# Kernel optimization log

Measured on AMD Instinct MI355X. Metric: run time of the kernel, lower is better.

## Reference

```python
import jax, jax.numpy as jnp
import numpy as np
import math

D_MODEL, N_HEADS, D_FF = 1024, 16, 4096
D_K = D_MODEL // N_HEADS
B, S = 4, 2048
EPS = 1e-5


def layer_norm(x, gamma, beta):
    mean = jnp.mean(x, axis=-1, keepdims=True)
    var = jnp.mean((x - mean) ** 2, axis=-1, keepdims=True)  # unbiased=False
    return gamma * (x - mean) / jnp.sqrt(var + EPS) + beta


def setup_inputs() -> dict:
    key = jax.random.key(0)
    ks = jax.random.split(key, 7)
    std_attn = math.sqrt(2.0 / (D_MODEL + D_MODEL))
    std_ff1 = math.sqrt(2.0 / (D_MODEL + D_FF))
    std_ff2 = math.sqrt(2.0 / (D_FF + D_MODEL))
    return {
        "x": jax.random.normal(ks[0], (B, S, D_MODEL), jnp.float32),
        "W_q": jax.random.normal(ks[1], (D_MODEL, D_MODEL), jnp.float32) * std_attn,
        "W_k": jax.random.normal(ks[2], (D_MODEL, D_MODEL), jnp.float32) * std_attn,
        "W_v": jax.random.normal(ks[3], (D_MODEL, D_MODEL), jnp.float32) * std_attn,
        "W_o": jax.random.normal(ks[4], (D_MODEL, D_MODEL), jnp.float32) * std_attn,
        "W1": jax.random.normal(ks[5], (D_MODEL, D_FF), jnp.float32) * std_ff1,
        "b1": jnp.zeros((D_FF,), jnp.float32),
        "W2": jax.random.normal(ks[6], (D_FF, D_MODEL), jnp.float32) * std_ff2,
        "b2": jnp.zeros((D_MODEL,), jnp.float32),
        "ln1_gamma": jnp.ones((D_MODEL,), jnp.float32),
        "ln1_beta": jnp.zeros((D_MODEL,), jnp.float32),
        "ln2_gamma": jnp.ones((D_MODEL,), jnp.float32),
        "ln2_beta": jnp.zeros((D_MODEL,), jnp.float32),
    }


def reference(x, W_q, W_k, W_v, W_o, W1, b1, W2, b2,
              ln1_gamma, ln1_beta, ln2_gamma, ln2_beta):
    b, s, d = x.shape
    # pre-LN attention block
    ln1 = layer_norm(x, ln1_gamma, ln1_beta)
    q = (ln1 @ W_q).reshape(b, s, N_HEADS, D_K)
    k = (ln1 @ W_k).reshape(b, s, N_HEADS, D_K)
    v = (ln1 @ W_v).reshape(b, s, N_HEADS, D_K)
    scores = jnp.einsum("bqhd,bkhd->bhqk", q, k) / math.sqrt(D_K)
    attn = jax.nn.softmax(scores, axis=-1)
    ctx = jnp.einsum("bhqk,bkhd->bqhd", attn, v).reshape(b, s, d)
    attn_out = ctx @ W_o
    attn_residual = x + attn_out
    # pre-LN FFN block
    ln2 = layer_norm(attn_residual, ln2_gamma, ln2_beta)
    ff = jax.nn.relu(ln2 @ W1 + b1) @ W2 + b2
    return attn_residual + ff
```

## Files before the change

kernel.cpp:

```cpp
#include <hip/hip_runtime.h>
#include <hip/hip_bf16.h>

typedef __attribute__((ext_vector_type(4))) float  floatx4;
typedef __attribute__((ext_vector_type(8))) short  shortx8;
typedef __attribute__((ext_vector_type(4))) short  shortx4;

__device__ __forceinline__ short f2bf(float f) {
    unsigned u = __float_as_uint(f);
    u += 0x7fffu + ((u >> 16) & 1u);
    return (short)(u >> 16);
}
__device__ __forceinline__ float bf2f(short s) {
    return __uint_as_float(((unsigned)(unsigned short)s) << 16);
}
__device__ __forceinline__ float fast_exp2(float x) {
#if __has_builtin(__builtin_amdgcn_exp2f)
    return __builtin_amdgcn_exp2f(x);
#else
    return exp2f(x);
#endif
}

__device__ __forceinline__ void load_lds16(const void* g, void* l) {
    __builtin_amdgcn_global_load_lds(
        (const __attribute__((address_space(1))) unsigned int*)g,
        (__attribute__((address_space(3))) unsigned int*)l,
        16, 0, 0);
}

__global__ __launch_bounds__(256)
void transpose_w(const float* __restrict__ src, short* __restrict__ dst, int K, int N)
{
    __shared__ __align__(16) float tile[32][33];
    const int n0 = blockIdx.x * 32, k0 = blockIdx.y * 32;
    const int tx = threadIdx.x & 31, ty = threadIdx.x >> 5;
    for (int i = 0; i < 32; i += 8)
        tile[ty + i][tx] = src[(size_t)(k0 + ty + i) * N + n0 + tx];
    __syncthreads();
    for (int i = 0; i < 32; i += 8)
        dst[(size_t)(n0 + ty + i) * K + k0 + tx] = f2bf(tile[tx][ty + i]);
}

__global__ __launch_bounds__(256)
void ln_bf16(const float* __restrict__ x, const float* __restrict__ g,
             const float* __restrict__ be, short* __restrict__ out)
{
    const int row = blockIdx.x;
    const int tid = threadIdx.x;
    const float4 v = reinterpret_cast<const float4*>(x + (size_t)row * 1024)[tid];
    float s  = v.x + v.y + v.z + v.w;
    float ss = v.x * v.x + v.y * v.y + v.z * v.z + v.w * v.w;
    for (int off = 32; off > 0; off >>= 1) {
        s  += __shfl_down(s,  off);
        ss += __shfl_down(ss, off);
    }
    __shared__ float rs[4], rss[4];
    const int wave = tid >> 6, lane = tid & 63;
    if (lane == 0) { rs[wave] = s; rss[wave] = ss; }
    __syncthreads();
    const float S    = rs[0] + rs[1] + rs[2] + rs[3];
    const float SS   = rss[0] + rss[1] + rss[2] + rss[3];
    const float mean = S * (1.0f / 1024.0f);
    const float var  = SS * (1.0f / 1024.0f) - mean * mean;
    const float rstd = rsqrtf(var + 1e-5f);
    const float4 gg = reinterpret_cast<const float4*>(g)[tid];
    const float4 bb = reinterpret_cast<const float4*>(be)[tid];
    shortx4 o;
    o[0] = f2bf(gg.x * ((v.x - mean) * rstd) + bb.x);
    o[1] = f2bf(gg.y * ((v.y - mean) * rstd) + bb.y);
    o[2] = f2bf(gg.z * ((v.z - mean) * rstd) + bb.z);
    o[3] = f2bf(gg.w * ((v.w - mean) * rstd) + bb.w);
    *reinterpret_cast<shortx4*>(out + (size_t)row * 1024 + tid * 4) = o;
}

template <int EPI>
__global__ __launch_bounds__(256)
void gemm_bt(const short* __restrict__ A, const short* __restrict__ Bt,
             short* __restrict__ Cb, float* __restrict__ Cf,
             const float* __restrict__ bias, const float* __restrict__ resid,
             int M, int N, int K)
{
    __shared__ __align__(16) short As[128 * 32];
    __shared__ __align__(16) short Bs[128 * 32];
    const int tid  = threadIdx.x;
    const int wave = tid >> 6;
    const int lane = tid & 63;
    const int quad = lane >> 4;
    const int l16  = lane & 15;
    const int wm = wave >> 1, wn = wave & 1;
    const size_t bm = (size_t)blockIdx.y * 128;
    const size_t bn = (size_t)blockIdx.x * 128;

    floatx4 acc[4][4];
    for (int i = 0; i < 4; i++)
        for (int j = 0; j < 4; j++)
            acc[i][j] = (floatx4){0.f, 0.f, 0.f, 0.f};

    const int c0 = wave * 2, c1 = wave * 2 + 1;
    const int rA0 = c0 * 16 + (lane >> 2);
    const int rA1 = c1 * 16 + (lane >> 2);
    const int colOff = (lane & 3) * 8;

    for (int k0 = 0; k0 < K; k0 += 32) {
        load_lds16(A  + (bm + rA0) * (size_t)K + k0 + colOff, &As[c0 * 512]);
        load_lds16(A  + (bm + rA1) * (size_t)K + k0 + colOff, &As[c1 * 512]);
        load_lds16(Bt + (bn + rA0) * (size_t)K + k0 + colOff, &Bs[c0 * 512]);
        load_lds16(Bt + (bn + rA1) * (size_t)K + k0 + colOff, &Bs[c1 * 512]);
        __syncthreads();
        shortx8 af[4], bf[4];
        for (int mi = 0; mi < 4; mi++)
            af[mi] = *(const shortx8*)&As[(wm * 64 + mi * 16 + l16) * 32 + quad * 8];
        for (int ni = 0; ni < 4; ni++)
            bf[ni] = *(const shortx8*)&Bs[(wn * 64 + ni * 16 + l16) * 32 + quad * 8];
        for (int mi = 0; mi < 4; mi++)
            for (int ni = 0; ni < 4; ni++)
                acc[mi][ni] = __builtin_amdgcn_mfma_f32_16x16x32_bf16(
                    af[mi], bf[ni], acc[mi][ni], 0, 0, 0);
        __syncthreads();
    }

    for (int mi = 0; mi < 4; mi++) {
        for (int ni = 0; ni < 4; ni++) {
            const size_t row0 = bm + wm * 64 + mi * 16 + quad * 4;
            const size_t col  = bn + wn * 64 + ni * 16 + l16;
            for (int r = 0; r < 4; r++) {
                float v = acc[mi][ni][r];
                const size_t idx = (row0 + r) * (size_t)N + col;
                if (EPI == 0) {
                    Cb[idx] = f2bf(v);
                } else if (EPI == 1) {
                    v += bias[col];
                    Cb[idx] = f2bf(v > 0.f ? v : 0.f);
                } else if (EPI == 2) {
                    Cf[idx] = resid[idx] + v;
                } else {
                    v += bias[col];
                    Cf[idx] = resid[idx] + v;
                }
            }
        }
    }
}

__global__ __launch_bounds__(256)
void transpose_v(const short* __restrict__ qkv, short* __restrict__ vt)
{
    __shared__ __align__(16) short tile[64][65];
    const int st = blockIdx.x, h = blockIdx.y, b = blockIdx.z;
    const int t = threadIdx.x;
    for (int i = 0; i < 2; i++) {
        const int idx = i * 256 + t;
        const int s = idx >> 3, dg = idx & 7;
        shortx8 val = *(const shortx8*)&qkv[(size_t)(b * 2048 + st * 64 + s) * 3072
                                           + 2048 + h * 64 + dg * 8];
        for (int u = 0; u < 8; u++) tile[s][dg * 8 + u] = val[u];
    }
    __syncthreads();
    const int d = t >> 2, sg = (t & 3) * 16;
    shortx8 lo, hi;
    for (int i = 0; i < 8; i++) {
        lo[i] = tile[sg + i][d];
        hi[i] = tile[sg + 8 + i][d];
    }
    const size_t base = ((size_t)(b * 16 + h) * 64 + d) * 2048 + st * 64 + sg;
    *(shortx8*)&vt[base]     = lo;
    *(shortx8*)&vt[base + 8] = hi;
}

__global__ __launch_bounds__(256)
void attention_kernel(const short* __restrict__ qkv, const short* __restrict__ vt,
                      short* __restrict__ ctx)
{
    const int qt = blockIdx.x, h = blockIdx.y, b = blockIdx.z;
    const int tid  = threadIdx.x;
    const int wave = tid >> 6;
    const int lane = tid & 63;
    const int quad = lane >> 4;
    const int l16  = lane & 15;

    __shared__ __align__(16) short Ks[64 * 72];
    __shared__ __align__(16) short Vs[80 * 72];
    __shared__ __align__(16) short Ps[4][16 * 72];

    for (int idx = tid; idx < 16 * 72; idx += 256)
        Vs[64 * 72 + idx] = (short)0x3F80;

    const int sq = qt * 64 + wave * 16 + l16;
    const short* qrow = qkv + (size_t)(b * 2048 + sq) * 3072 + h * 64;
    const float qscale = 0.125f * 1.44269504088896f;
    shortx8 qf[2];
    for (int kk = 0; kk < 2; kk++) {
        shortx8 raw = *(const shortx8*)&qrow[kk * 32 + quad * 8];
        for (int j = 0; j < 8; j++) raw[j] = f2bf(bf2f(raw[j]) * qscale);
        qf[kk] = raw;
    }

    floatx4 accO[5];
    for (int dt = 0; dt < 5; dt++) accO[dt] = (floatx4){0.f, 0.f, 0.f, 0.f};

    const short* kbase = qkv + (size_t)(b * 2048) * 3072 + 1024 + h * 64;
    const short* vbase = vt + ((size_t)(b * 16 + h) * 64) * 2048;

    for (int kt = 0; kt < 32; ++kt) {
        __syncthreads();
        for (int i = 0; i < 2; i++) {
            const int idx = i * 256 + tid;
            const int s = idx >> 3, dg = idx & 7;
            shortx8 kv = *(const shortx8*)&kbase[(size_t)(kt * 64 + s) * 3072 + dg * 8];
            *(shortx8*)&Ks[s * 72 + dg * 8] = kv;
            shortx8 vv = *(const shortx8*)&vbase[(size_t)s * 2048 + kt * 64 + dg * 8];
            *(shortx8*)&Vs[s * 72 + dg * 8] = vv;
        }
        __syncthreads();

        floatx4 st[4];
        for (int nt = 0; nt < 4; nt++) {
            floatx4 c = (floatx4){0.f, 0.f, 0.f, 0.f};
            for (int kk = 0; kk < 2; kk++) {
                shortx8 kf = *(const shortx8*)&Ks[(nt * 16 + l16) * 72 + kk * 32 + quad * 8];
                c = __builtin_amdgcn_mfma_f32_16x16x32_bf16(kf, qf[kk], c, 0, 0, 0);
            }
            st[nt] = c;
        }

        for (int nt = 0; nt < 4; nt++) {
            float2 p01, p23;
            p01.x = fast_exp2(st[nt][0]);
            p01.y = fast_exp2(st[nt][1]);
            p23.x = fast_exp2(st[nt][2]);
            p23.y = fast_exp2(st[nt][3]);
            union { __hip_bfloat162 h2[2]; uint2 u; } pk;
            pk.h2[0] = __float22bfloat162_rn(p01);
            pk.h2[1] = __float22bfloat162_rn(p23);
            *(uint2*)&Ps[wave][l16 * 72 + nt * 16 + quad * 4] = pk.u;
        }
        asm volatile("s_waitcnt lgkmcnt(0)" ::: "memory");

        shortx8 pf0 = *(const shortx8*)&Ps[wave][l16 * 72 + 0 * 32 + quad * 8];
        shortx8 pf1 = *(const shortx8*)&Ps[wave][l16 * 72 + 1 * 32 + quad * 8];

        for (int dt = 0; dt < 5; dt++) {
            floatx4 c = accO[dt];
            shortx8 vf0 = *(const shortx8*)&Vs[(dt * 16 + l16) * 72 + 0 * 32 + quad * 8];
            shortx8 vf1 = *(const shortx8*)&Vs[(dt * 16 + l16) * 72 + 1 * 32 + quad * 8];
            c = __builtin_amdgcn_mfma_f32_16x16x32_bf16(pf0, vf0, c, 0, 0, 0);
            c = __builtin_amdgcn_mfma_f32_16x16x32_bf16(pf1, vf1, c, 0, 0, 0);
            accO[dt] = c;
        }
    }

    const int qg = qt * 64 + wave * 16 + quad * 4;
    for (int r = 0; r < 4; r++) {
        const float inv = 1.0f / accO[4][r];
        for (int dt = 0; dt < 4; dt++)
            ctx[(size_t)(b * 2048 + qg + r) * 1024 + h * 64 + dt * 16 + l16]
                = f2bf(accO[dt][r] * inv);
    }
}

extern "C" void kernel_launch(void* const* d_in, const int* in_sizes, int n_in,
                              void* d_out, int out_size, void* d_ws, size_t ws_size,
                              hipStream_t stream)
{
    const float* x   = (const float*)d_in[0];
    const float* Wq  = (const float*)d_in[1];
    const float* Wk  = (const float*)d_in[2];
    const float* Wv  = (const float*)d_in[3];
    const float* Wo  = (const float*)d_in[4];
    const float* W1  = (const float*)d_in[5];
    const float* b1  = (const float*)d_in[6];
    const float* W2  = (const float*)d_in[7];
    const float* b2  = (const float*)d_in[8];
    const float* g1  = (const float*)d_in[9];
    const float* be1 = (const float*)d_in[10];
    const float* g2  = (const float*)d_in[11];
    const float* be2 = (const float*)d_in[12];
    float* out = (float*)d_out;
    char*  ws  = (char*)d_ws;

    const size_t MiB = 1u << 20;
    short* regA   = (short*)(ws);
    short* qkv    = (short*)(ws + 16 * MiB);
    short* vt     = (short*)(ws + 64 * MiB);
    short* ff1    = qkv;
    short* Wqkv_t = (short*)(ws + 80 * MiB);
    short* Wo_t   = (short*)(ws + 86 * MiB);
    short* W1_t   = (short*)(ws + 88 * MiB);
    short* W2_t   = (short*)(ws + 96 * MiB);

    const dim3 blk(256);

    transpose_w<<<dim3(32, 32),  blk, 0, stream>>>(Wq, Wqkv_t,                  1024, 1024);
    transpose_w<<<dim3(32, 32),  blk, 0, stream>>>(Wk, Wqkv_t + 1024 * 1024,    1024, 1024);
    transpose_w<<<dim3(32, 32),  blk, 0, stream>>>(Wv, Wqkv_t + 2 * 1024 * 1024,1024, 1024);
    transpose_w<<<dim3(32, 32),  blk, 0, stream>>>(Wo, Wo_t,                    1024, 1024);
    transpose_w<<<dim3(128, 32), blk, 0, stream>>>(W1, W1_t,                    1024, 4096);
    transpose_w<<<dim3(32, 128), blk, 0, stream>>>(W2, W2_t,                    4096, 1024);

    ln_bf16<<<8192, blk, 0, stream>>>(x, g1, be1, regA);
    gemm_bt<0><<<dim3(24, 64), blk, 0, stream>>>(regA, Wqkv_t, qkv, nullptr, nullptr, nullptr,
                                                 8192, 3072, 1024);
    transpose_v<<<dim3(32, 16, 4), blk, 0, stream>>>(qkv, vt);
    attention_kernel<<<dim3(32, 16, 4), blk, 0, stream>>>(qkv, vt, regA);
    gemm_bt<2><<<dim3(8, 64), blk, 0, stream>>>(regA, Wo_t, nullptr, out, nullptr, x,
                                                8192, 1024, 1024);
    ln_bf16<<<8192, blk, 0, stream>>>(out, g2, be2, regA);
    gemm_bt<1><<<dim3(32, 64), blk, 0, stream>>>(regA, W1_t, ff1, nullptr, b1, nullptr,
                                                 8192, 4096, 1024);
    gemm_bt<3><<<dim3(8, 64), blk, 0, stream>>>(ff1, W2_t, nullptr, out, b2, out,
                                                8192, 1024, 4096);
}
```

Baseline: 619.1 us.

## Process two query tiles per wave in attention to reuse K/V fragments

Each wave now handles 32 query rows instead of 16, so the attention block covers 128 queries and the grid's query dimension is halved. Every K and V fragment loaded from shared memory feeds two MFMAs, which halves the K/V global-to-LDS traffic per query and raises MFMA density. The cost is roughly doubled accumulator and score registers, which may lower occupancy. The grid shrinks to 1024 blocks, leaving fewer blocks to hide latency.

```diff
diff --git a/kernel.cpp b/kernel.cpp
--- a/kernel.cpp
+++ b/kernel.cpp
@@ -180,23 +180,26 @@
 
     __shared__ __align__(16) short Ks[64 * 72];
     __shared__ __align__(16) short Vs[80 * 72];
-    __shared__ __align__(16) short Ps[4][16 * 72];
+    __shared__ __align__(16) short Ps[4][32 * 72];
 
     for (int idx = tid; idx < 16 * 72; idx += 256)
         Vs[64 * 72 + idx] = (short)0x3F80;
 
-    const int sq = qt * 64 + wave * 16 + l16;
-    const short* qrow = qkv + (size_t)(b * 2048 + sq) * 3072 + h * 64;
+    const int q0 = qt * 128 + wave * 32;
     const float qscale = 0.125f * 1.44269504088896f;
-    shortx8 qf[2];
-    for (int kk = 0; kk < 2; kk++) {
-        shortx8 raw = *(const shortx8*)&qrow[kk * 32 + quad * 8];
-        for (int j = 0; j < 8; j++) raw[j] = f2bf(bf2f(raw[j]) * qscale);
-        qf[kk] = raw;
-    }
-
-    floatx4 accO[5];
-    for (int dt = 0; dt < 5; dt++) accO[dt] = (floatx4){0.f, 0.f, 0.f, 0.f};
+    shortx8 qf[2][2];
+    for (int qi = 0; qi < 2; qi++) {
+        const short* qrow = qkv + (size_t)(b * 2048 + q0 + qi * 16 + l16) * 3072 + h * 64;
+        for (int kk = 0; kk < 2; kk++) {
+            shortx8 raw = *(const shortx8*)&qrow[kk * 32 + quad * 8];
+            for (int j = 0; j < 8; j++) raw[j] = f2bf(bf2f(raw[j]) * qscale);
+            qf[qi][kk] = raw;
+        }
+    }
+
+    floatx4 accO[2][5];
+    for (int qi = 0; qi < 2; qi++)
+        for (int dt = 0; dt < 5; dt++) accO[qi][dt] = (floatx4){0.f, 0.f, 0.f, 0.f};
 
     const short* kbase = qkv + (size_t)(b * 2048) * 3072 + 1024 + h * 64;
     const short* vbase = vt + ((size_t)(b * 16 + h) * 64) * 2048;
@@ -213,48 +216,57 @@
         }
         __syncthreads();
 
-        floatx4 st[4];
+        floatx4 st[4][2];
         for (int nt = 0; nt < 4; nt++) {
-            floatx4 c = (floatx4){0.f, 0.f, 0.f, 0.f};
-            for (int kk = 0; kk < 2; kk++) {
-                shortx8 kf = *(const shortx8*)&Ks[(nt * 16 + l16) * 72 + kk * 32 + quad * 8];
-                c = __builtin_amdgcn_mfma_f32_16x16x32_bf16(kf, qf[kk], c, 0, 0, 0);
+            shortx8 kf0 = *(const shortx8*)&Ks[(nt * 16 + l16) * 72 + 0 * 32 + quad * 8];
+            shortx8 kf1 = *(const shortx8*)&Ks[(nt * 16 + l16) * 72 + 1 * 32 + quad * 8];
+            for (int qi = 0; qi < 2; qi++) {
+                floatx4 c = (floatx4){0.f, 0.f, 0.f, 0.f};
+                c = __builtin_amdgcn_mfma_f32_16x16x32_bf16(kf0, qf[qi][0], c, 0, 0, 0);
+                c = __builtin_amdgcn_mfma_f32_16x16x32_bf16(kf1, qf[qi][1], c, 0, 0, 0);
+                st[nt][qi] = c;
             }
-            st[nt] = c;
-        }
-
-        for (int nt = 0; nt < 4; nt++) {
-            float2 p01, p23;
-            p01.x = fast_exp2(st[nt][0]);
-            p01.y = fast_exp2(st[nt][1]);
-            p23.x = fast_exp2(st[nt][2]);
-            p23.y = fast_exp2(st[nt][3]);
-            union { __hip_bfloat162 h2[2]; uint2 u; } pk;
-            pk.h2[0] = __float22bfloat162_rn(p01);
-            pk.h2[1] = __float22bfloat162_rn(p23);
-            *(uint2*)&Ps[wave][l16 * 72 + nt * 16 + quad * 4] = pk.u;
-        }
+        }
+
+        for (int nt = 0; nt < 4; nt++)
+            for (int qi = 0; qi < 2; qi++) {
+                float2 p01, p23;
+                p01.x = fast_exp2(st[nt][qi][0]);
+                p01.y = fast_exp2(st[nt][qi][1]);
+                p23.x = fast_exp2(st[nt][qi][2]);
+                p23.y = fast_exp2(st[nt][qi][3]);
+                union { __hip_bfloat162 h2[2]; uint2 u; } pk;
+                pk.h2[0] = __float22bfloat162_rn(p01);
+                pk.h2[1] = __float22bfloat162_rn(p23);
+                *(uint2*)&Ps[wave][(qi * 16 + l16) * 72 + nt * 16 + quad * 4] = pk.u;
+            }
         asm volatile("s_waitcnt lgkmcnt(0)" ::: "memory");
 
-        shortx8 pf0 = *(const shortx8*)&Ps[wave][l16 * 72 + 0 * 32 + quad * 8];
-        shortx8 pf1 = *(const shortx8*)&Ps[wave][l16 * 72 + 1 * 32 + quad * 8];
+        shortx8 pf[2][2];
+        for (int qi = 0; qi < 2; qi++)
+            for (int kk = 0; kk < 2; kk++)
+                pf[qi][kk] = *(const shortx8*)&Ps[wave][(qi * 16 + l16) * 72 + kk * 32 + quad * 8];
 
         for (int dt = 0; dt < 5; dt++) {
-            floatx4 c = accO[dt];
             shortx8 vf0 = *(const shortx8*)&Vs[(dt * 16 + l16) * 72 + 0 * 32 + quad * 8];
             shortx8 vf1 = *(const shortx8*)&Vs[(dt * 16 + l16) * 72 + 1 * 32 + quad * 8];
-            c = __builtin_amdgcn_mfma_f32_16x16x32_bf16(pf0, vf0, c, 0, 0, 0);
-            c = __builtin_amdgcn_mfma_f32_16x16x32_bf16(pf1, vf1, c, 0, 0, 0);
-            accO[dt] = c;
-        }
-    }
-
-    const int qg = qt * 64 + wave * 16 + quad * 4;
-    for (int r = 0; r < 4; r++) {
-        const float inv = 1.0f / accO[4][r];
-        for (int dt = 0; dt < 4; dt++)
-            ctx[(size_t)(b * 2048 + qg + r) * 1024 + h * 64 + dt * 16 + l16]
-                = f2bf(accO[dt][r] * inv);
+            for (int qi = 0; qi < 2; qi++) {
+                floatx4 c = accO[qi][dt];
+                c = __builtin_amdgcn_mfma_f32_16x16x32_bf16(pf[qi][0], vf0, c, 0, 0, 0);
+                c = __builtin_amdgcn_mfma_f32_16x16x32_bf16(pf[qi][1], vf1, c, 0, 0, 0);
+                accO[qi][dt] = c;
+            }
+        }
+    }
+
+    for (int qi = 0; qi < 2; qi++) {
+        const int qg = q0 + qi * 16 + quad * 4;
+        for (int r = 0; r < 4; r++) {
+            const float inv = 1.0f / accO[qi][4][r];
+            for (int dt = 0; dt < 4; dt++)
+                ctx[(size_t)(b * 2048 + qg + r) * 1024 + h * 64 + dt * 16 + l16]
+                    = f2bf(accO[qi][dt][r] * inv);
+        }
     }
 }
 
@@ -301,7 +313,7 @@
     gemm_bt<0><<<dim3(24, 64), blk, 0, stream>>>(regA, Wqkv_t, qkv, nullptr, nullptr, nullptr,
                                                  8192, 3072, 1024);
     transpose_v<<<dim3(32, 16, 4), blk, 0, stream>>>(qkv, vt);
-    attention_kernel<<<dim3(32, 16, 4), blk, 0, stream>>>(qkv, vt, regA);
+    attention_kernel<<<dim3(16, 16, 4), blk, 0, stream>>>(qkv, vt, regA);
     gemm_bt<2><<<dim3(8, 64), blk, 0, stream>>>(regA, Wo_t, nullptr, out, nullptr, x,
                                                 8192, 1024, 1024);
     ln_bf16<<<8192, blk, 0, stream>>>(out, g2, be2, regA);
```

Result: no change. 630.3 us (+1.8%).

## Use 512-thread attention blocks covering 128 queries and keep ones vector in registers

Applied to the files above, without the earlier changes.

The attention kernel now runs 8 waves per block over 128 query rows instead of 4 waves over 64, so each K/V tile staged in LDS is shared by twice as many queries and the grid halves. Each thread loads a single K and V vector per tile. The row-sum ones column previously held in LDS is replaced by a register constant fed directly to the MFMA, which shrinks the V buffer and removes those LDS reads. Larger blocks may reduce occupancy flexibility and leave fewer blocks to spread across CUs.

```diff
diff --git a/kernel.cpp b/kernel.cpp
--- a/kernel.cpp
+++ b/kernel.cpp
@@ -167,7 +167,7 @@
     *(shortx8*)&vt[base + 8] = hi;
 }
 
-__global__ __launch_bounds__(256)
+__global__ __launch_bounds__(512)
 void attention_kernel(const short* __restrict__ qkv, const short* __restrict__ vt,
                       short* __restrict__ ctx)
 {
@@ -179,15 +179,12 @@
     const int l16  = lane & 15;
 
     __shared__ __align__(16) short Ks[64 * 72];
-    __shared__ __align__(16) short Vs[80 * 72];
-    __shared__ __align__(16) short Ps[4][16 * 72];
-
-    for (int idx = tid; idx < 16 * 72; idx += 256)
-        Vs[64 * 72 + idx] = (short)0x3F80;
-
-    const int sq = qt * 64 + wave * 16 + l16;
-    const short* qrow = qkv + (size_t)(b * 2048 + sq) * 3072 + h * 64;
+    __shared__ __align__(16) short Vs[64 * 72];
+    __shared__ __align__(16) short Ps[8][16 * 72];
+
+    const int q0 = qt * 128 + wave * 16;
     const float qscale = 0.125f * 1.44269504088896f;
+    const short* qrow = qkv + (size_t)(b * 2048 + q0 + l16) * 3072 + h * 64;
     shortx8 qf[2];
     for (int kk = 0; kk < 2; kk++) {
         shortx8 raw = *(const shortx8*)&qrow[kk * 32 + quad * 8];
@@ -195,31 +192,35 @@
         qf[kk] = raw;
     }
 
+    shortx8 vones;
+    for (int j = 0; j < 8; j++) vones[j] = (short)0x3F80;
+
     floatx4 accO[5];
     for (int dt = 0; dt < 5; dt++) accO[dt] = (floatx4){0.f, 0.f, 0.f, 0.f};
 
     const short* kbase = qkv + (size_t)(b * 2048) * 3072 + 1024 + h * 64;
     const short* vbase = vt + ((size_t)(b * 16 + h) * 64) * 2048;
+    short* const psw = &Ps[wave][0];
+
+    const int ss = tid >> 3, sdg = tid & 7;
 
     for (int kt = 0; kt < 32; ++kt) {
         __syncthreads();
-        for (int i = 0; i < 2; i++) {
-            const int idx = i * 256 + tid;
-            const int s = idx >> 3, dg = idx & 7;
-            shortx8 kv = *(const shortx8*)&kbase[(size_t)(kt * 64 + s) * 3072 + dg * 8];
-            *(shortx8*)&Ks[s * 72 + dg * 8] = kv;
-            shortx8 vv = *(const shortx8*)&vbase[(size_t)s * 2048 + kt * 64 + dg * 8];
-            *(shortx8*)&Vs[s * 72 + dg * 8] = vv;
+        {
+            shortx8 kv = *(const shortx8*)&kbase[(size_t)(kt * 64 + ss) * 3072 + sdg * 8];
+            *(shortx8*)&Ks[ss * 72 + sdg * 8] = kv;
+            shortx8 vv = *(const shortx8*)&vbase[(size_t)ss * 2048 + kt * 64 + sdg * 8];
+            *(shortx8*)&Vs[ss * 72 + sdg * 8] = vv;
         }
         __syncthreads();
 
         floatx4 st[4];
         for (int nt = 0; nt < 4; nt++) {
+            shortx8 kf0 = *(const shortx8*)&Ks[(nt * 16 + l16) * 72 + 0 * 32 + quad * 8];
+            shortx8 kf1 = *(const shortx8*)&Ks[(nt * 16 + l16) * 72 + 1 * 32 + quad * 8];
             floatx4 c = (floatx4){0.f, 0.f, 0.f, 0.f};
-            for (int kk = 0; kk < 2; kk++) {
-                shortx8 kf = *(const shortx8*)&Ks[(nt * 16 + l16) * 72 + kk * 32 + quad * 8];
-                c = __builtin_amdgcn_mfma_f32_16x16x32_bf16(kf, qf[kk], c, 0, 0, 0);
-            }
+            c = __builtin_amdgcn_mfma_f32_16x16x32_bf16(kf0, qf[0], c, 0, 0, 0);
+            c = __builtin_amdgcn_mfma_f32_16x16x32_bf16(kf1, qf[1], c, 0, 0, 0);
             st[nt] = c;
         }
 
@@ -232,24 +233,30 @@
             union { __hip_bfloat162 h2[2]; uint2 u; } pk;
             pk.h2[0] = __float22bfloat162_rn(p01);
             pk.h2[1] = __float22bfloat162_rn(p23);
-            *(uint2*)&Ps[wave][l16 * 72 + nt * 16 + quad * 4] = pk.u;
+            *(uint2*)&psw[l16 * 72 + nt * 16 + quad * 4] = pk.u;
         }
         asm volatile("s_waitcnt lgkmcnt(0)" ::: "memory");
 
-        shortx8 pf0 = *(const shortx8*)&Ps[wave][l16 * 72 + 0 * 32 + quad * 8];
-        shortx8 pf1 = *(const shortx8*)&Ps[wave][l16 * 72 + 1 * 32 + quad * 8];
-
-        for (int dt = 0; dt < 5; dt++) {
-            floatx4 c = accO[dt];
+        shortx8 pf0 = *(const shortx8*)&psw[l16 * 72 + 0 * 32 + quad * 8];
+        shortx8 pf1 = *(const shortx8*)&psw[l16 * 72 + 1 * 32 + quad * 8];
+
+        for (int dt = 0; dt < 4; dt++) {
             shortx8 vf0 = *(const shortx8*)&Vs[(dt * 16 + l16) * 72 + 0 * 32 + quad * 8];
             shortx8 vf1 = *(const shortx8*)&Vs[(dt * 16 + l16) * 72 + 1 * 32 + quad * 8];
+            floatx4 c = accO[dt];
             c = __builtin_amdgcn_mfma_f32_16x16x32_bf16(pf0, vf0, c, 0, 0, 0);
             c = __builtin_amdgcn_mfma_f32_16x16x32_bf16(pf1, vf1, c, 0, 0, 0);
             accO[dt] = c;
         }
-    }
-
-    const int qg = qt * 64 + wave * 16 + quad * 4;
+        {
+            floatx4 c = accO[4];
+            c = __builtin_amdgcn_mfma_f32_16x16x32_bf16(pf0, vones, c, 0, 0, 0);
+            c = __builtin_amdgcn_mfma_f32_16x16x32_bf16(pf1, vones, c, 0, 0, 0);
+            accO[4] = c;
+        }
+    }
+
+    const int qg = q0 + quad * 4;
     for (int r = 0; r < 4; r++) {
         const float inv = 1.0f / accO[4][r];
         for (int dt = 0; dt < 4; dt++)
@@ -301,7 +308,7 @@
     gemm_bt<0><<<dim3(24, 64), blk, 0, stream>>>(regA, Wqkv_t, qkv, nullptr, nullptr, nullptr,
                                                  8192, 3072, 1024);
     transpose_v<<<dim3(32, 16, 4), blk, 0, stream>>>(qkv, vt);
-    attention_kernel<<<dim3(32, 16, 4), blk, 0, stream>>>(qkv, vt, regA);
+    attention_kernel<<<dim3(16, 16, 4), dim3(512), 0, stream>>>(qkv, vt, regA);
     gemm_bt<2><<<dim3(8, 64), blk, 0, stream>>>(regA, Wo_t, nullptr, out, nullptr, x,
                                                 8192, 1024, 1024);
     ln_bf16<<<8192, blk, 0, stream>>>(out, g2, be2, regA);
```

Result: faster. 585.8 us (-5.4%).
